# Kernel tuning notes

Hardware: AMD Instinct MI355X
Metric: run time of the kernel (lower is better)

Reference implementation:

```python
import jax, jax.numpy as jnp
import numpy as np

H = 16  # number of heads

def setup_inputs() -> dict:
    key = jax.random.key(0)
    ks = jax.random.split(key, 8)
    B, T, D = 4, 2048, 1024
    s = 0.02
    return {
        "query": jax.random.normal(ks[0], (B, T, D), jnp.float32),
        "key":   jax.random.normal(ks[1], (B, T, D), jnp.float32),
        "value": jax.random.normal(ks[2], (B, T, D), jnp.float32),
        "mask":  jnp.ones((B, T, T), jnp.int32),
        # torch nn.Linear weights: [out_features, in_features]
        "Wq": jax.random.normal(ks[3], (D, D), jnp.float32) * s,
        "Wk": jax.random.normal(ks[4], (D, D), jnp.float32) * s,
        "Wv": jax.random.normal(ks[5], (D, D), jnp.float32) * s,
        "Wo": jax.random.normal(ks[6], (D, D), jnp.float32) * s,
        "bo": jnp.zeros((D,), jnp.float32),
    }

def reference(query, key, value, mask, Wq, Wk, Wv, Wo, bo):
    B, Tq, _ = query.shape
    Tk = key.shape[1]
    Dv = Wv.shape[0]
    # linear projections (y = x @ W^T), split into heads: [B, H, T, dh]
    Q = jnp.einsum('btd,ed->bte', query, Wq).reshape(B, Tq, H, -1).transpose(0, 2, 1, 3)
    K = jnp.einsum('btd,ed->bte', key,   Wk).reshape(B, Tk, H, -1).transpose(0, 2, 1, 3)
    V = jnp.einsum('btd,ed->bte', value, Wv).reshape(B, Tk, H, -1).transpose(0, 2, 1, 3)
    d_k = K.shape[-1]
    scores = jnp.einsum('bhqd,bhkd->bhqk', Q, K) / jnp.sqrt(jnp.asarray(d_k, Q.dtype))
    # mask broadcast: [B,1,Tq,Tk]; masked_fill(mask==0, -1e9)
    scores = jnp.where(mask[:, None] == 0, jnp.asarray(-1e9, scores.dtype), scores)
    attn = jax.nn.softmax(scores, axis=-1)
    Z = jnp.einsum('bhqk,bhkd->bhqd', attn, V)          # [B,H,Tq,dh]
    Zc = Z.transpose(0, 2, 1, 3).reshape(B, Tq, Dv)     # concat heads
    return jnp.einsum('btd,ed->bte', Zc, Wo) + bo
```

## Files before the change

kernel.cpp:

```cpp
#include <hip/hip_runtime.h>

typedef __bf16 bf16x8 __attribute__((ext_vector_type(8)));
typedef float f32x4 __attribute__((ext_vector_type(4)));
typedef unsigned short u16;
typedef unsigned long long u64;

#define NX 8388608
#define NW 1048576

__device__ __forceinline__ u16 f2bf(float f) {
  union { float f; unsigned u; } c; c.f = f;
  unsigned u = c.u;
  u += 0x7fffu + ((u >> 16) & 1u);
  return (u16)(u >> 16);
}

__device__ __forceinline__ f32x4 mfma16(bf16x8 a, bf16x8 b, f32x4 c) {
  return __builtin_amdgcn_mfma_f32_16x16x32_bf16(a, b, c, 0, 0, 0);
}

__device__ __forceinline__ void gld16(void* lds, const void* g) {
  __builtin_amdgcn_global_load_lds(
      (const __attribute__((address_space(1))) unsigned int*)g,
      (__attribute__((address_space(3))) unsigned int*)lds, 16, 0, 0);
}

__global__ __launch_bounds__(256) void cast_all(
    const float* __restrict__ q, const float* __restrict__ k,
    const float* __restrict__ v, const float* __restrict__ wq,
    const float* __restrict__ wk, const float* __restrict__ wv,
    const float* __restrict__ wo, u16* __restrict__ xbf, u16* __restrict__ wbf) {
  long long i = ((long long)blockIdx.x * 256 + threadIdx.x) * 8;
  const float* src; u16* dst; long long off;
  if (i < (long long)NX)            { src = q; dst = xbf;            off = i; }
  else if (i < 2LL * NX)            { src = k; dst = xbf + NX;       off = i - NX; }
  else if (i < 3LL * NX)            { src = v; dst = xbf + 2LL * NX; off = i - 2LL * NX; }
  else {
    long long j = i - 3LL * NX;
    int w = (int)(j / NW); off = j - (long long)w * NW;
    src = (w == 0) ? wq : (w == 1) ? wk : (w == 2) ? wv : wo;
    dst = wbf + (long long)w * NW;
  }
  float4 a = *(const float4*)(src + off);
  float4 b = *(const float4*)(src + off + 4);
  u16 o[8] = {f2bf(a.x), f2bf(a.y), f2bf(a.z), f2bf(a.w),
              f2bf(b.x), f2bf(b.y), f2bf(b.z), f2bf(b.w)};
  *(uint4*)(dst + off) = *(const uint4*)o;
}

__global__ __launch_bounds__(256) void mask_pack(
    const int* __restrict__ mask, u64* __restrict__ bits) {
  const int row = blockIdx.x * 4 + (threadIdx.x >> 6);
  const int lane = threadIdx.x & 63;
  const int* mrow = mask + (long long)row * 2048;
#pragma unroll
  for (int it = 0; it < 32; it++) {
    u64 w = __ballot(mrow[it * 64 + lane] != 0);
    if (lane == 0) bits[row * 32 + it] = w;
  }
}

template <int MODE>
__global__ __launch_bounds__(256, 2) void gemm128(
    const u16* __restrict__ Abase, const u16* __restrict__ Wbase,
    u16* __restrict__ oq, u16* __restrict__ ok, u16* __restrict__ ovt,
    const float* __restrict__ bias, float* __restrict__ of) {
  __shared__ u16 smem[2][128 * 64];
  u16* sA = smem[0];
  u16* sB = smem[1];
  const u16* A = Abase;
  const u16* W = Wbase;
  if (MODE == 0) { A += (long long)blockIdx.z * NX; W += (long long)blockIdx.z * NW; }
  const int tid = threadIdx.x, wave = tid >> 6, lane = tid & 63;
  const int quad = lane >> 4, l15 = lane & 15;
  const int m0 = blockIdx.y * 128, n0 = blockIdx.x * 128;
  const int wm = (wave & 1) * 64, wn = (wave >> 1) * 64;
  const int lr = lane >> 3;
  const int gc = (lane & 7) ^ lr;
  f32x4 acc[4][4];
#pragma unroll
  for (int i = 0; i < 4; i++)
#pragma unroll
    for (int j = 0; j < 4; j++) acc[i][j] = (f32x4){0.f, 0.f, 0.f, 0.f};

  for (int ks = 0; ks < 16; ks++) {
    const int k0 = ks * 64;
    __syncthreads();
#pragma unroll
    for (int t = 0; t < 4; t++) {
      const int rb = wave * 32 + t * 8;
      gld16(&sA[rb * 64], &A[(m0 + rb + lr) * 1024 + k0 + gc * 8]);
      gld16(&sB[rb * 64], &W[(n0 + rb + lr) * 1024 + k0 + gc * 8]);
    }
    __syncthreads();
#pragma unroll
    for (int kc = 0; kc < 2; kc++) {
      bf16x8 aF[4], bF[4];
#pragma unroll
      for (int i = 0; i < 4; i++)
        aF[i] = *(const bf16x8*)&sA[(wm + 16 * i + l15) * 64 +
                                    (((kc * 4 + quad) ^ (l15 & 7)) * 8)];
#pragma unroll
      for (int j = 0; j < 4; j++)
        bF[j] = *(const bf16x8*)&sB[(wn + 16 * j + l15) * 64 +
                                    (((kc * 4 + quad) ^ (l15 & 7)) * 8)];
#pragma unroll
      for (int i = 0; i < 4; i++)
#pragma unroll
        for (int j = 0; j < 4; j++) acc[i][j] = mfma16(aF[i], bF[j], acc[i][j]);
    }
  }

  if (MODE == 0) {
    const int z = blockIdx.z;
    if (z < 2) {
      const float qscale = (z == 0) ? 0.18033688f : 1.0f;
      u16* dst = (z == 0) ? oq : ok;
#pragma unroll
      for (int i = 0; i < 4; i++)
#pragma unroll
        for (int j = 0; j < 4; j++)
#pragma unroll
          for (int r = 0; r < 4; r++) {
            int m = m0 + wm + 16 * i + quad * 4 + r;
            int n = n0 + wn + 16 * j + l15;
            int b = m >> 11, t = m & 2047, h = n >> 6, d = n & 63;
            dst[(((b << 4) + h) * 2048 + t) * 64 + d] = f2bf(acc[i][j][r] * qscale);
          }
    } else {
      __syncthreads();
      u16* sT = &smem[0][0] + wave * 4096;
#pragma unroll
      for (int i = 0; i < 4; i++)
#pragma unroll
        for (int j = 0; j < 4; j++)
#pragma unroll
          for (int r = 0; r < 4; r++) {
            int m = 16 * i + quad * 4 + r;
            int n = 16 * j + l15;
            sT[n * 64 + (((m >> 3) ^ (n & 7)) * 8) + (m & 7)] = f2bf(acc[i][j][r]);
          }
      const int b = m0 >> 11, t0 = (m0 + wm) & 2047;
      const int h = (n0 + wn) >> 6;
      u16* dst = ovt + ((long long)((b << 4) + h)) * 131072 + lane * 2048 + t0;
#pragma unroll
      for (int c = 0; c < 8; c++) {
        uint4 val = *(const uint4*)&sT[lane * 64 + ((c ^ (lane & 7)) * 8)];
        *(uint4*)(dst + c * 8) = val;
      }
    }
  } else {
    float bb[4];
#pragma unroll
    for (int j = 0; j < 4; j++) bb[j] = bias[n0 + wn + 16 * j + l15];
#pragma unroll
    for (int i = 0; i < 4; i++)
#pragma unroll
      for (int j = 0; j < 4; j++)
#pragma unroll
        for (int r = 0; r < 4; r++) {
          int m = m0 + wm + 16 * i + quad * 4 + r;
          int n = n0 + wn + 16 * j + l15;
          of[m * 1024 + n] = acc[i][j][r] + bb[j];
        }
  }
}

__global__ __launch_bounds__(256, 2) void attn(
    const u16* __restrict__ Qh, const u16* __restrict__ Kh,
    const u16* __restrict__ Vt, const u64* __restrict__ mbits,
    u16* __restrict__ Zc) {
  __shared__ u16 sK[128 * 64];
  __shared__ u16 sV[64 * 128];
  __shared__ alignas(16) u16 sP[4][32][136];
  const int tid = threadIdx.x, wave = tid >> 6, lane = tid & 63;
  const int quad = lane >> 4, l15 = lane & 15;
  const int bh = blockIdx.y, b = bh >> 4, h = bh & 15, qt = blockIdx.x;
  const int q0 = qt * 128 + wave * 32;
  const int lr8 = lane >> 3, gc8 = (lane & 7) ^ (lr8 & 7);
  const int lr4 = lane >> 4, lc16 = lane & 15;

  bf16x8 qa[2][2];
#pragma unroll
  for (int g = 0; g < 2; g++)
#pragma unroll
    for (int kc = 0; kc < 2; kc++)
      qa[g][kc] = *(const bf16x8*)&Qh[(bh * 2048 + q0 + g * 16 + l15) * 64 +
                                      kc * 32 + quad * 8];

  const u64* mb[2];
#pragma unroll
  for (int g = 0; g < 2; g++)
    mb[g] = mbits + (long long)(b * 2048 + q0 + g * 16 + quad * 4) * 32;

  f32x4 oacc[2][4];
#pragma unroll
  for (int g = 0; g < 2; g++)
#pragma unroll
    for (int j = 0; j < 4; j++) oacc[g][j] = (f32x4){0.f, 0.f, 0.f, 0.f};
  float lv[2][4] = {{0.f, 0.f, 0.f, 0.f}, {0.f, 0.f, 0.f, 0.f}};

  for (int kt = 0; kt < 16; kt++) {
    __syncthreads();
#pragma unroll
    for (int t = 0; t < 4; t++) {
      const int rbk = wave * 32 + t * 8;
      const int kap = (((rbk & 15) + lr8) << 3) + (rbk >> 4);
      gld16(&sK[rbk * 64], &Kh[(bh * 2048 + kt * 128 + kap) * 64 + gc8 * 8]);
      const int rbv = wave * 16 + t * 4;
      gld16(&sV[rbv * 128],
            &Vt[(bh * 64 + rbv + lr4) * 2048 + kt * 128 + ((lc16 ^ (t * 4 + lr4)) * 8)]);
    }
    u64 mw[2][4][2];
#pragma unroll
    for (int g = 0; g < 2; g++)
#pragma unroll
      for (int r = 0; r < 4; r++) {
        mw[g][r][0] = mb[g][r * 32 + 2 * kt];
        mw[g][r][1] = mb[g][r * 32 + 2 * kt + 1];
      }
    __syncthreads();

    f32x4 sacc[2][8];
#pragma unroll
    for (int g = 0; g < 2; g++)
#pragma unroll
      for (int j = 0; j < 8; j++) sacc[g][j] = (f32x4){0.f, 0.f, 0.f, 0.f};
#pragma unroll
    for (int kc = 0; kc < 2; kc++)
#pragma unroll
      for (int j = 0; j < 8; j++) {
        bf16x8 kF = *(const bf16x8*)&sK[(16 * j + l15) * 64 +
                                        (((kc * 4 + quad) ^ (l15 & 7)) * 8)];
        sacc[0][j] = mfma16(qa[0][kc], kF, sacc[0][j]);
        sacc[1][j] = mfma16(qa[1][kc], kF, sacc[1][j]);
      }

    u64 allm = ~0ull;
#pragma unroll
    for (int g = 0; g < 2; g++)
#pragma unroll
      for (int r = 0; r < 4; r++) allm &= mw[g][r][0] & mw[g][r][1];
    bool full = __all(allm == ~0ull);
    if (full) {
#pragma unroll
      for (int g = 0; g < 2; g++)
#pragma unroll
        for (int r = 0; r < 4; r++) {
          bf16x8 pk;
          float ls = 0.f;
#pragma unroll
          for (int j = 0; j < 8; j++) {
            float p = __builtin_amdgcn_exp2f(sacc[g][j][r]);
            ls += p;
            pk[j] = (__bf16)p;
          }
          lv[g][r] += ls;
          *(bf16x8*)&sP[wave][g * 16 + quad * 4 + r][l15 * 8] = pk;
        }
    } else {
#pragma unroll
      for (int g = 0; g < 2; g++)
#pragma unroll
        for (int r = 0; r < 4; r++) {
          bf16x8 pk;
          float ls = 0.f;
          u64 w = mw[g][r][l15 >> 3];
#pragma unroll
          for (int j = 0; j < 8; j++) {
            float p = __builtin_amdgcn_exp2f(sacc[g][j][r]);
            p = ((w >> (((l15 & 7) << 3) + j)) & 1ull) ? p : 0.f;
            ls += p;
            pk[j] = (__bf16)p;
          }
          lv[g][r] += ls;
          *(bf16x8*)&sP[wave][g * 16 + quad * 4 + r][l15 * 8] = pk;
        }
    }

#pragma unroll
    for (int kc = 0; kc < 4; kc++) {
      bf16x8 aP0 = *(const bf16x8*)&sP[wave][l15][kc * 32 + quad * 8];
      bf16x8 aP1 = *(const bf16x8*)&sP[wave][16 + l15][kc * 32 + quad * 8];
#pragma unroll
      for (int j = 0; j < 4; j++) {
        bf16x8 vF = *(const bf16x8*)&sV[(16 * j + l15) * 128 +
                                        (((kc * 4 + quad) ^ l15) * 8)];
        oacc[0][j] = mfma16(aP0, vF, oacc[0][j]);
        oacc[1][j] = mfma16(aP1, vF, oacc[1][j]);
      }
    }
  }

#pragma unroll
  for (int g = 0; g < 2; g++) {
    float inv[4];
#pragma unroll
    for (int r = 0; r < 4; r++) {
      float s = lv[g][r];
      s += __shfl_xor(s, 1);
      s += __shfl_xor(s, 2);
      s += __shfl_xor(s, 4);
      s += __shfl_xor(s, 8);
      inv[r] = 1.f / s;
    }
#pragma unroll
    for (int j = 0; j < 4; j++)
#pragma unroll
      for (int r = 0; r < 4; r++) {
        int t = q0 + g * 16 + quad * 4 + r;
        Zc[(b * 2048 + t) * 1024 + h * 64 + 16 * j + l15] =
            f2bf(oacc[g][j][r] * inv[r]);
      }
  }
}

extern "C" void kernel_launch(void* const* d_in, const int* in_sizes, int n_in,
                              void* d_out, int out_size, void* d_ws, size_t ws_size,
                              hipStream_t stream) {
  (void)in_sizes; (void)n_in; (void)out_size; (void)ws_size;
  const float* q    = (const float*)d_in[0];
  const float* k    = (const float*)d_in[1];
  const float* v    = (const float*)d_in[2];
  const int*   mask = (const int*)d_in[3];
  const float* Wq   = (const float*)d_in[4];
  const float* Wk   = (const float*)d_in[5];
  const float* Wv   = (const float*)d_in[6];
  const float* Wo   = (const float*)d_in[7];
  const float* bo   = (const float*)d_in[8];
  float* out = (float*)d_out;

  u16* Xbf = (u16*)d_ws;
  u16* Wbf = Xbf + 3LL * NX;
  u16* Qh  = Wbf + 4LL * NW;
  u16* Kh  = Qh + (long long)NX;
  u16* Vt  = Kh + (long long)NX;
  u16* Zc  = Vt + (long long)NX;
  u64* Mb  = (u64*)(Zc + (long long)NX);

  cast_all<<<14336, 256, 0, stream>>>(q, k, v, Wq, Wk, Wv, Wo, Xbf, Wbf);
  mask_pack<<<2048, 256, 0, stream>>>(mask, Mb);
  gemm128<0><<<dim3(8, 64, 3), 256, 0, stream>>>(Xbf, Wbf, Qh, Kh, Vt, nullptr, nullptr);
  attn<<<dim3(16, 64), 256, 0, stream>>>(Qh, Kh, Vt, Mb, Zc);
  gemm128<1><<<dim3(8, 64), 256, 0, stream>>>(Zc, Wbf + 3LL * NW, nullptr, nullptr, nullptr,
                                              bo, out);
}
```

Before: 396.3 us.

## Double-buffer attention K/V tiles with 64-key steps and hoisted mask check

Shrinks the attention key tile from 128 to 64 and double-buffers the K and V shared-memory tiles, so the next tile's global-to-LDS load is issued before the current tile is computed, with one barrier per iteration instead of two. The mask-all-ones test now runs once per block up front, which skips the per-tile mask loads on fully unmasked rows. Block IDs are remapped to reorder work across heads, and occupancy is raised to 3 blocks per CU. The cost is twice as many loop iterations, a tighter register budget, and less MFMA work per barrier.

Result: no change. 390.5 us (-1.5%).

```diff
diff --git a/kernel.cpp b/kernel.cpp
--- a/kernel.cpp
+++ b/kernel.cpp
@@ -1,6 +1,7 @@
 #include <hip/hip_runtime.h>
 
 typedef __bf16 bf16x8 __attribute__((ext_vector_type(8)));
+typedef __bf16 bf16x4 __attribute__((ext_vector_type(4)));
 typedef float f32x4 __attribute__((ext_vector_type(4)));
 typedef unsigned short u16;
 typedef unsigned long long u64;
@@ -166,19 +167,34 @@
   }
 }
 
-__global__ __launch_bounds__(256, 2) void attn(
+__device__ __forceinline__ void stage_tile(
+    u16* sKb, u16* sVb, const u16* __restrict__ Kh, const u16* __restrict__ Vt,
+    int bh, int kt, int wave, int lr8, int gc8) {
+#pragma unroll
+  for (int t = 0; t < 2; t++) {
+    const int rb = wave * 16 + t * 8;
+    const int c = rb + lr8;
+    const int kap = ((c & 15) << 2) + (c >> 4);
+    gld16(&sKb[rb * 64], &Kh[(bh * 2048 + kt * 64 + kap) * 64 + gc8 * 8]);
+    gld16(&sVb[rb * 64], &Vt[(bh * 64 + rb + lr8) * 2048 + kt * 64 + gc8 * 8]);
+  }
+}
+
+__global__ __launch_bounds__(256, 3) void attn(
     const u16* __restrict__ Qh, const u16* __restrict__ Kh,
     const u16* __restrict__ Vt, const u64* __restrict__ mbits,
     u16* __restrict__ Zc) {
-  __shared__ u16 sK[128 * 64];
-  __shared__ u16 sV[64 * 128];
-  __shared__ alignas(16) u16 sP[4][32][136];
+  __shared__ u16 sK[2][64 * 64];
+  __shared__ u16 sV[2][64 * 64];
+  __shared__ alignas(16) u16 sP[4][32][72];
   const int tid = threadIdx.x, wave = tid >> 6, lane = tid & 63;
   const int quad = lane >> 4, l15 = lane & 15;
-  const int bh = blockIdx.y, b = bh >> 4, h = bh & 15, qt = blockIdx.x;
+  const int id = blockIdx.y * 16 + blockIdx.x;
+  const int id2 = (id & 7) * 128 + (id >> 3);
+  const int bh = id2 >> 4, qt = id2 & 15;
+  const int b = bh >> 4, h = bh & 15;
   const int q0 = qt * 128 + wave * 32;
-  const int lr8 = lane >> 3, gc8 = (lane & 7) ^ (lr8 & 7);
-  const int lr4 = lane >> 4, lc16 = lane & 15;
+  const int lr8 = lane >> 3, gc8 = (lane & 7) ^ lr8;
 
   bf16x8 qa[2][2];
 #pragma unroll
@@ -188,6 +204,12 @@
       qa[g][kc] = *(const bf16x8*)&Qh[(bh * 2048 + q0 + g * 16 + l15) * 64 +
                                       kc * 32 + quad * 8];
 
+  const u64* mrow = mbits + (long long)(b * 2048 + q0) * 32;
+  u64 am = ~0ull;
+#pragma unroll
+  for (int i = 0; i < 16; i++) am &= mrow[lane * 16 + i];
+  const bool allfull = __all(am == ~0ull);
+
   const u64* mb[2];
 #pragma unroll
   for (int g = 0; g < 2; g++)
@@ -200,92 +222,82 @@
     for (int j = 0; j < 4; j++) oacc[g][j] = (f32x4){0.f, 0.f, 0.f, 0.f};
   float lv[2][4] = {{0.f, 0.f, 0.f, 0.f}, {0.f, 0.f, 0.f, 0.f}};
 
-  for (int kt = 0; kt < 16; kt++) {
+  stage_tile(&sK[0][0], &sV[0][0], Kh, Vt, bh, 0, wave, lr8, gc8);
+
+  for (int kt = 0; kt < 32; kt++) {
+    const int cur = kt & 1;
     __syncthreads();
-#pragma unroll
-    for (int t = 0; t < 4; t++) {
-      const int rbk = wave * 32 + t * 8;
-      const int kap = (((rbk & 15) + lr8) << 3) + (rbk >> 4);
-      gld16(&sK[rbk * 64], &Kh[(bh * 2048 + kt * 128 + kap) * 64 + gc8 * 8]);
-      const int rbv = wave * 16 + t * 4;
-      gld16(&sV[rbv * 128],
-            &Vt[(bh * 64 + rbv + lr4) * 2048 + kt * 128 + ((lc16 ^ (t * 4 + lr4)) * 8)]);
-    }
-    u64 mw[2][4][2];
+
+    u64 mw[2][4];
+    if (!allfull) {
+#pragma unroll
+      for (int g = 0; g < 2; g++)
+#pragma unroll
+        for (int r = 0; r < 4; r++) mw[g][r] = mb[g][r * 32 + kt];
+    }
+    if (kt < 31)
+      stage_tile(&sK[cur ^ 1][0], &sV[cur ^ 1][0], Kh, Vt, bh, kt + 1,
+                 wave, lr8, gc8);
+
+    f32x4 sacc[2][4];
 #pragma unroll
     for (int g = 0; g < 2; g++)
 #pragma unroll
-      for (int r = 0; r < 4; r++) {
-        mw[g][r][0] = mb[g][r * 32 + 2 * kt];
-        mw[g][r][1] = mb[g][r * 32 + 2 * kt + 1];
-      }
-    __syncthreads();
-
-    f32x4 sacc[2][8];
-#pragma unroll
-    for (int g = 0; g < 2; g++)
-#pragma unroll
-      for (int j = 0; j < 8; j++) sacc[g][j] = (f32x4){0.f, 0.f, 0.f, 0.f};
+      for (int j = 0; j < 4; j++) sacc[g][j] = (f32x4){0.f, 0.f, 0.f, 0.f};
 #pragma unroll
     for (int kc = 0; kc < 2; kc++)
 #pragma unroll
-      for (int j = 0; j < 8; j++) {
-        bf16x8 kF = *(const bf16x8*)&sK[(16 * j + l15) * 64 +
-                                        (((kc * 4 + quad) ^ (l15 & 7)) * 8)];
+      for (int j = 0; j < 4; j++) {
+        bf16x8 kF = *(const bf16x8*)&sK[cur][(16 * j + l15) * 64 +
+                                            (((kc * 4 + quad) ^ (l15 & 7)) * 8)];
         sacc[0][j] = mfma16(qa[0][kc], kF, sacc[0][j]);
         sacc[1][j] = mfma16(qa[1][kc], kF, sacc[1][j]);
       }
 
-    u64 allm = ~0ull;
-#pragma unroll
-    for (int g = 0; g < 2; g++)
-#pragma unroll
-      for (int r = 0; r < 4; r++) allm &= mw[g][r][0] & mw[g][r][1];
-    bool full = __all(allm == ~0ull);
-    if (full) {
+    if (allfull) {
 #pragma unroll
       for (int g = 0; g < 2; g++)
 #pragma unroll
         for (int r = 0; r < 4; r++) {
-          bf16x8 pk;
+          bf16x4 pk;
           float ls = 0.f;
 #pragma unroll
-          for (int j = 0; j < 8; j++) {
+          for (int j = 0; j < 4; j++) {
             float p = __builtin_amdgcn_exp2f(sacc[g][j][r]);
             ls += p;
             pk[j] = (__bf16)p;
           }
           lv[g][r] += ls;
-          *(bf16x8*)&sP[wave][g * 16 + quad * 4 + r][l15 * 8] = pk;
+          *(bf16x4*)&sP[wave][g * 16 + quad * 4 + r][l15 * 4] = pk;
         }
     } else {
 #pragma unroll
       for (int g = 0; g < 2; g++)
 #pragma unroll
         for (int r = 0; r < 4; r++) {
-          bf16x8 pk;
+          bf16x4 pk;
           float ls = 0.f;
-          u64 w = mw[g][r][l15 >> 3];
-#pragma unroll
-          for (int j = 0; j < 8; j++) {
+          u64 w = mw[g][r];
+#pragma unroll
+          for (int j = 0; j < 4; j++) {
             float p = __builtin_amdgcn_exp2f(sacc[g][j][r]);
-            p = ((w >> (((l15 & 7) << 3) + j)) & 1ull) ? p : 0.f;
+            p = ((w >> (l15 * 4 + j)) & 1ull) ? p : 0.f;
             ls += p;
             pk[j] = (__bf16)p;
           }
           lv[g][r] += ls;
-          *(bf16x8*)&sP[wave][g * 16 + quad * 4 + r][l15 * 8] = pk;
+          *(bf16x4*)&sP[wave][g * 16 + quad * 4 + r][l15 * 4] = pk;
         }
     }
 
 #pragma unroll
-    for (int kc = 0; kc < 4; kc++) {
+    for (int kc = 0; kc < 2; kc++) {
       bf16x8 aP0 = *(const bf16x8*)&sP[wave][l15][kc * 32 + quad * 8];
       bf16x8 aP1 = *(const bf16x8*)&sP[wave][16 + l15][kc * 32 + quad * 8];
 #pragma unroll
       for (int j = 0; j < 4; j++) {
-        bf16x8 vF = *(const bf16x8*)&sV[(16 * j + l15) * 128 +
-                                        (((kc * 4 + quad) ^ l15) * 8)];
+        bf16x8 vF = *(const bf16x8*)&sV[cur][(16 * j + l15) * 64 +
+                                            (((kc * 4 + quad) ^ (l15 & 7)) * 8)];
         oacc[0][j] = mfma16(aP0, vF, oacc[0][j]);
         oacc[1][j] = mfma16(aP1, vF, oacc[1][j]);
       }
```
